# Optimization experiments

Measured on AMD Instinct MI355X. Metric: run time of the kernel, lower is better.

The kernel has to match this reference:

```python
import jax, jax.numpy as jnp
import numpy as np

RCR, RCA = 5.1, 3.5
ETA_R, ZETA, ETA_A = 19.7, 14.1, 12.5
SHF_R = jnp.asarray((0.8 + 0.26875 * np.arange(16)).astype(np.float32))   # 16 radial shifts
SHF_Z = jnp.asarray(((2 * np.arange(8) + 1) * np.pi / 8).astype(np.float32))  # 8 angle shifts
SHF_A = jnp.asarray((0.8 + 0.3375 * np.arange(8)).astype(np.float32))    # 8 angular-radial shifts
NUM_SPECIES = 7
NUM_PAIRS = NUM_SPECIES * (NUM_SPECIES + 1) // 2  # 28 unordered species pairs
N = 2000          # atoms
K = 24            # max neighbors considered for angular terms (Rca=3.5 -> ~18 at this density)
BOX = 27.1        # (N / 0.1 atoms/A^3)^(1/3)

def _triu_index(n):
    ret = np.zeros((n, n), dtype=np.int32)
    iu = np.triu_indices(n)
    ret[iu] = np.arange(iu[0].size)
    ret[iu[1], iu[0]] = ret[iu]
    return ret
TRIU = jnp.asarray(_triu_index(NUM_SPECIES))  # [7,7] -> pair index in 0..27

def _fc(d, rc):
    # cosine cutoff, zero beyond rc
    return jnp.where(d <= rc, 0.5 * jnp.cos(jnp.pi * d / rc) + 0.5, 0.0)

def setup_inputs():
    key = jax.random.key(0)
    k1, k2 = jax.random.split(key)
    species = jax.random.randint(k1, (N,), 0, NUM_SPECIES)
    positions = jax.random.uniform(k2, (N, 3), dtype=jnp.float32) * BOX
    return {"species": species, "positions": positions}

def _aev_mean(species, positions):
    n = positions.shape[0]
    eye = jnp.eye(n, dtype=bool)
    diff = positions[:, None, :] - positions[None, :, :]          # [n,n,3]
    d2 = jnp.sum(diff * diff, -1)
    dist = jnp.sqrt(jnp.where(eye, 1.0, d2))                      # safe sqrt on diagonal
    dist = jnp.where(eye, 2.0 * RCR, dist)                        # exclude self (fc -> 0)

    # ---- radial AEV: 0.25 * exp(-EtaR (d - ShfR)^2) * fc(d, Rcr), scattered by neighbor species
    fc_r = _fc(dist, RCR)
    rad = 0.25 * jnp.exp(-ETA_R * (dist[..., None] - SHF_R) ** 2) * fc_r[..., None]  # [n,n,16]
    oh = jax.nn.one_hot(species, NUM_SPECIES, dtype=positions.dtype)                  # [n,7]
    radial = jnp.einsum('ijr,js->isr', rad, oh)                   # [n,7,16]

    # ---- angular AEV over triplets (j, i, k) with j,k among K nearest neighbors of i
    neg, idx = jax.lax.top_k(-dist, K)                            # idx: [n,K]
    nd = -neg                                                     # neighbor distances [n,K]
    valid = nd <= RCA
    vec = positions[idx] - positions[:, None, :]                  # [n,K,3]
    rj = nd[:, :, None]
    rk = nd[:, None, :]
    cos_ang = 0.95 * jnp.einsum('nad,nbd->nab', vec, vec) / (rj * rk)  # torchani's 0.95 factor
    theta = jnp.arccos(cos_ang)                                   # [n,K,K]
    f1 = ((1.0 + jnp.cos(theta[..., None] - SHF_Z)) / 2.0) ** ZETA               # [n,K,K,8]
    f2 = jnp.exp(-ETA_A * (((rj + rk) / 2.0)[..., None] - SHF_A) ** 2)           # [n,K,K,8]
    fcj = _fc(nd, RCA)
    tri = jnp.triu(jnp.ones((K, K), dtype=bool), 1)               # unordered pairs j<k
    mask = valid[:, :, None] & valid[:, None, :] & tri
    pref = 2.0 * fcj[:, :, None] * fcj[:, None, :] * mask.astype(positions.dtype)
    g = (f1[..., :, None] * f2[..., None, :]).reshape(n, K, K, 64) * pref[..., None]  # [n,K,K,64]
    sp_nb = species[idx]                                          # [n,K]
    pair_idx = TRIU[sp_nb[:, :, None], sp_nb[:, None, :]]         # [n,K,K] in 0..27
    row = jnp.arange(n)[:, None, None]
    angular = jnp.zeros((n, NUM_PAIRS, 64), dtype=positions.dtype).at[row, pair_idx].add(g)

    aev = jnp.concatenate([radial.reshape(n, -1), angular.reshape(n, -1)], axis=-1)  # [n,1904]
    return jnp.mean(aev)

def reference(species, positions):
    return _aev_mean(species, positions)
```

## Files before the change

### kernel.cpp

```cpp
#include <hip/hip_runtime.h>
#include <math.h>

#define NATOMS 2000
#define KNBR   24
#define BLOCK  256
#define NWAVE  4
#define WHCAP  48
#define WACAP  24
#define NFEAT  1904.0f

__device__ __forceinline__ float wave_reduce_add(float v) {
    #pragma unroll
    for (int off = 32; off > 0; off >>= 1) v += __shfl_down(v, off, 64);
    return v;
}

__device__ __forceinline__ int mask_rank_below(unsigned long long m) {
    return (int)__builtin_amdgcn_mbcnt_hi((unsigned)(m >> 32),
                 __builtin_amdgcn_mbcnt_lo((unsigned)m, 0u));
}

__global__ __launch_bounds__(BLOCK) void aev_block_kernel(
        const float* __restrict__ pos, float* __restrict__ partial) {
    constexpr float RCR = 5.1f, RCA = 3.5f;
    constexpr float ETA_R = 19.7f, ZETA = 14.1f, ETA_A = 12.5f;
    constexpr float PI = 3.14159265358979323846f;

    __shared__ float hd2[NWAVE][WHCAP];
    __shared__ int   hj [NWAVE][WHCAP];
    __shared__ float ad [NWAVE][WACAP];
    __shared__ int   aj [NWAVE][WACAP];
    __shared__ int   acnt[NWAVE];
    __shared__ float nbx[KNBR], nby[KNBR], nbz[KNBR], nbd[KNBR], nbfc[KNBR];
    __shared__ float red[NWAVE];

    const int tid  = threadIdx.x;
    const int w    = tid >> 6;
    const int lane = tid & 63;
    const int i    = blockIdx.x;

    const float xi = pos[3 * i + 0], yi = pos[3 * i + 1], zi = pos[3 * i + 2];

    int hbase = 0;
    #pragma unroll 4
    for (int it = 0; it < 8; it++) {
        int j  = w * 64 + it * 256 + lane;
        int jc = j < NATOMS ? j : 0;
        float dx = pos[3 * jc + 0] - xi;
        float dy = pos[3 * jc + 1] - yi;
        float dz = pos[3 * jc + 2] - zi;
        float d2 = dx * dx + dy * dy + dz * dz;
        bool hit = (j < NATOMS) && (j != i) && (d2 <= RCR * RCR);
        unsigned long long m = __ballot(hit);
        if (hit) {
            int idx = hbase + mask_rank_below(m);
            if (idx < WHCAP) { hd2[w][idx] = d2; hj[w][idx] = j; }
        }
        hbase += __popcll(m);
    }

    int hcnt = min(hbase, WHCAP);
    float rsum = 0.0f;
    float d = 0.0f, d2v = 1e9f;
    bool act = lane < hcnt;
    {
        int cl = min(lane, WHCAP - 1);
        if (act) d2v = hd2[w][cl];
        if (act) {
            d = sqrtf(d2v);
            float fc = 0.5f * __cosf(d * (PI / RCR)) + 0.5f;
            float s = 0.0f;
            #pragma unroll
            for (int r = 0; r < 16; r++) {
                float t = d - (0.8f + 0.26875f * (float)r);
                s += __expf(-ETA_R * t * t);
            }
            rsum = 0.25f * fc * s;
        }
        bool ahit = act && (d2v <= RCA * RCA);
        unsigned long long m = __ballot(ahit);
        if (ahit) {
            int idx = mask_rank_below(m);
            if (idx < WACAP) { ad[w][idx] = d; aj[w][idx] = hj[w][min(lane, WHCAP - 1)]; }
        }
        if (lane == 0) acnt[w] = min((int)__popcll(m), WACAP);
    }
    __syncthreads();

    int c0 = acnt[0], c1 = acnt[1], c2 = acnt[2], c3 = acnt[3];
    int cnt = min(c0 + c1 + c2 + c3, 64);
    int M   = min(cnt, KNBR);
    if (tid < cnt) {
        int t = tid, seg = 0;
        if (t >= c0) { t -= c0; seg = 1;
            if (t >= c1) { t -= c1; seg = 2;
                if (t >= c2) { t -= c2; seg = 3; } } }
        float dt = ad[seg][t];
        int   jt = aj[seg][t];
        int rank = 0;
        for (int s = 0; s < NWAVE; s++) {
            int cs = acnt[s];
            for (int u = 0; u < cs; u++) {
                float du = ad[s][u];
                if (du < dt || (du == dt && aj[s][u] < jt)) rank++;
            }
        }
        if (rank < KNBR) {
            nbx[rank]  = pos[3 * jt + 0] - xi;
            nby[rank]  = pos[3 * jt + 1] - yi;
            nbz[rank]  = pos[3 * jt + 2] - zi;
            nbd[rank]  = dt;
            nbfc[rank] = 0.5f * __cosf(dt * (PI / RCA)) + 0.5f;
        }
    }
    __syncthreads();

    const float CZ[4] = { 0.92387953251f, 0.38268343236f, -0.38268343236f, -0.92387953251f };
    const float SZ[4] = { 0.38268343236f, 0.92387953251f,  0.92387953251f,  0.38268343236f };
    float asum = 0.0f;
    int npairs = M * (M - 1) / 2;
    for (int p = tid; p < npairs; p += BLOCK) {
        int a = 0, rem = p;
        while (rem >= M - 1 - a) { rem -= M - 1 - a; a++; }
        int b = a + 1 + rem;

        float ra = nbd[a], rb = nbd[b];
        float dot = nbx[a] * nbx[b] + nby[a] * nby[b] + nbz[a] * nbz[b];
        float ca = 0.95f * dot / (ra * rb);
        float sa = sqrtf(fmaxf(0.0f, 1.0f - ca * ca));

        float f1 = 0.0f;
        #pragma unroll
        for (int z = 0; z < 4; z++) {
            float g = 0.5f * (ca * CZ[z] + sa * SZ[z]);
            f1 += __powf(fmaxf(0.5f + g, 1e-20f), ZETA);
            f1 += __powf(fmaxf(0.5f - g, 1e-20f), ZETA);
        }
        float avg = 0.5f * (ra + rb);
        float f2  = 0.0f;
        #pragma unroll
        for (int s8 = 0; s8 < 8; s8++) {
            float t = avg - (0.8f + 0.3375f * (float)s8);
            f2 += __expf(-ETA_A * t * t);
        }
        asum += 2.0f * nbfc[a] * nbfc[b] * f1 * f2;
    }

    float psum = wave_reduce_add(rsum + asum);
    if (lane == 0) red[w] = psum;
    __syncthreads();
    if (tid == 0) {
        float total = 0.0f;
        #pragma unroll
        for (int q = 0; q < NWAVE; q++) total += red[q];
        partial[i] = total;
    }
}

__global__ __launch_bounds__(BLOCK) void finalize_kernel(
        const float* __restrict__ partial, float* __restrict__ out) {
    __shared__ float red[BLOCK / 64];
    const int tid = threadIdx.x;
    float v = 0.0f;
    for (int c = tid; c < NATOMS; c += BLOCK) v += partial[c];
    v = wave_reduce_add(v);
    if ((tid & 63) == 0) red[tid >> 6] = v;
    __syncthreads();
    if (tid == 0) {
        float total = 0.0f;
        #pragma unroll
        for (int q = 0; q < BLOCK / 64; q++) total += red[q];
        out[0] = total / ((float)NATOMS * NFEAT);
    }
}

extern "C" void kernel_launch(void* const* d_in, const int* in_sizes, int n_in,
                              void* d_out, int out_size, void* d_ws, size_t ws_size,
                              hipStream_t stream) {
    const float* pos = (const float*)d_in[1];
    float* partial = (float*)d_ws;

    aev_block_kernel<<<NATOMS, BLOCK, 0, stream>>>(pos, partial);
    finalize_kernel<<<1, BLOCK, 0, stream>>>(partial, (float*)d_out);
}
```

Baseline: 79.87 us.

## Split neighbor scan into separate wave-parallel kernel with global atomic hit lists

Moves the all-pairs distance scan out of the per-atom block into its own kernel, where eight waves per atom each scan a 256-atom slice and append hits to a global per-atom list through atomics. The AEV kernel then reads the compacted hit list, uses one block-wide list instead of per-wave segments, and ranks angular neighbors over a single array. The intent is to raise parallelism in the scan and simplify the ranking. The cost is an extra memset, an extra launch, and a global round-trip of the hit data. Neighbor order within the hit list now depends on atomic ordering, but ranking breaks ties by index, so the chosen set stays deterministic.

```diff
diff --git a/kernel.cpp b/kernel.cpp
--- a/kernel.cpp
+++ b/kernel.cpp
@@ -4,10 +4,15 @@
 #define NATOMS 2000
 #define KNBR   24
 #define BLOCK  256
-#define NWAVE  4
-#define WHCAP  48
-#define WACAP  24
-#define NFEAT  1904.0f
+#define HCAP   128
+#define ACAP   64
+#define NSUB   8
+#define INV_SCALE (1.0f / (2000.0f * 1904.0f))
+
+__device__ __forceinline__ int mask_rank_below(unsigned long long m) {
+    return (int)__builtin_amdgcn_mbcnt_hi((unsigned)(m >> 32),
+                 __builtin_amdgcn_mbcnt_lo((unsigned)m, 0u));
+}
 
 __device__ __forceinline__ float wave_reduce_add(float v) {
     #pragma unroll
@@ -15,36 +20,21 @@
     return v;
 }
 
-__device__ __forceinline__ int mask_rank_below(unsigned long long m) {
-    return (int)__builtin_amdgcn_mbcnt_hi((unsigned)(m >> 32),
-                 __builtin_amdgcn_mbcnt_lo((unsigned)m, 0u));
-}
-
-__global__ __launch_bounds__(BLOCK) void aev_block_kernel(
-        const float* __restrict__ pos, float* __restrict__ partial) {
-    constexpr float RCR = 5.1f, RCA = 3.5f;
-    constexpr float ETA_R = 19.7f, ZETA = 14.1f, ETA_A = 12.5f;
-    constexpr float PI = 3.14159265358979323846f;
-
-    __shared__ float hd2[NWAVE][WHCAP];
-    __shared__ int   hj [NWAVE][WHCAP];
-    __shared__ float ad [NWAVE][WACAP];
-    __shared__ int   aj [NWAVE][WACAP];
-    __shared__ int   acnt[NWAVE];
-    __shared__ float nbx[KNBR], nby[KNBR], nbz[KNBR], nbd[KNBR], nbfc[KNBR];
-    __shared__ float red[NWAVE];
-
-    const int tid  = threadIdx.x;
-    const int w    = tid >> 6;
-    const int lane = tid & 63;
-    const int i    = blockIdx.x;
+__global__ __launch_bounds__(BLOCK) void scan_kernel(
+        const float* __restrict__ pos, int* __restrict__ cnt,
+        float2* __restrict__ hits) {
+    constexpr float RCR = 5.1f;
+    const int lane = threadIdx.x & 63;
+    int wid = blockIdx.x * (BLOCK / 64) + (threadIdx.x >> 6);
+    wid = __builtin_amdgcn_readfirstlane(wid);
+    const int i   = wid >> 3;
+    const int sub = wid & 7;
 
     const float xi = pos[3 * i + 0], yi = pos[3 * i + 1], zi = pos[3 * i + 2];
 
-    int hbase = 0;
-    #pragma unroll 4
-    for (int it = 0; it < 8; it++) {
-        int j  = w * 64 + it * 256 + lane;
+    #pragma unroll
+    for (int q = 0; q < 4; q++) {
+        int j  = sub * 256 + q * 64 + lane;
         int jc = j < NATOMS ? j : 0;
         float dx = pos[3 * jc + 0] - xi;
         float dy = pos[3 * jc + 1] - yi;
@@ -52,24 +42,51 @@
         float d2 = dx * dx + dy * dy + dz * dz;
         bool hit = (j < NATOMS) && (j != i) && (d2 <= RCR * RCR);
         unsigned long long m = __ballot(hit);
+        int nw = __popcll(m);
+        int base = 0;
+        if (lane == 0 && nw) base = atomicAdd(&cnt[i], nw);
+        base = __shfl(base, 0, 64);
         if (hit) {
-            int idx = hbase + mask_rank_below(m);
-            if (idx < WHCAP) { hd2[w][idx] = d2; hj[w][idx] = j; }
-        }
-        hbase += __popcll(m);
-    }
-
-    int hcnt = min(hbase, WHCAP);
+            int idx = base + mask_rank_below(m);
+            if (idx < HCAP)
+                hits[i * HCAP + idx] = make_float2(sqrtf(d2), __int_as_float(j));
+        }
+    }
+}
+
+__global__ __launch_bounds__(BLOCK) void aev_kernel(
+        const float* __restrict__ pos, const int* __restrict__ cnt,
+        const float2* __restrict__ hits, float* __restrict__ partial) {
+    constexpr float RCR = 5.1f, RCA = 3.5f;
+    constexpr float ETA_R = 19.7f, ZETA = 14.1f, ETA_A = 12.5f;
+    constexpr float PI = 3.14159265358979323846f;
+
+    __shared__ float ad[ACAP];
+    __shared__ int   aj[ACAP];
+    __shared__ int   s_acnt;
+    __shared__ float nbx[KNBR], nby[KNBR], nbz[KNBR], nbd[KNBR], nbfc[KNBR];
+    __shared__ float red[BLOCK / 64];
+
+    const int tid  = threadIdx.x;
+    const int lane = tid & 63;
+    const int i    = blockIdx.x;
+
+    if (tid == 0) s_acnt = 0;
+    __syncthreads();
+
+    const float xi = pos[3 * i + 0], yi = pos[3 * i + 1], zi = pos[3 * i + 2];
+    const int hcnt = min(cnt[i], HCAP);
+
     float rsum = 0.0f;
-    float d = 0.0f, d2v = 1e9f;
-    bool act = lane < hcnt;
     {
-        int cl = min(lane, WHCAP - 1);
-        if (act) d2v = hd2[w][cl];
+        bool act = tid < hcnt;
+        float d = 1.0e9f; int jv = 0;
         if (act) {
-            d = sqrtf(d2v);
+            float2 h = hits[i * HCAP + tid];
+            d  = h.x;
+            jv = __float_as_int(h.y);
             float fc = 0.5f * __cosf(d * (PI / RCR)) + 0.5f;
-            float s = 0.0f;
+            float s  = 0.0f;
             #pragma unroll
             for (int r = 0; r < 16; r++) {
                 float t = d - (0.8f + 0.26875f * (float)r);
@@ -77,33 +94,28 @@
             }
             rsum = 0.25f * fc * s;
         }
-        bool ahit = act && (d2v <= RCA * RCA);
+        bool ahit = act && (d <= RCA);
         unsigned long long m = __ballot(ahit);
+        int nw = __popcll(m);
+        int base = 0;
+        if (lane == 0 && nw) base = atomicAdd(&s_acnt, nw);
+        base = __shfl(base, 0, 64);
         if (ahit) {
-            int idx = mask_rank_below(m);
-            if (idx < WACAP) { ad[w][idx] = d; aj[w][idx] = hj[w][min(lane, WHCAP - 1)]; }
-        }
-        if (lane == 0) acnt[w] = min((int)__popcll(m), WACAP);
-    }
-    __syncthreads();
-
-    int c0 = acnt[0], c1 = acnt[1], c2 = acnt[2], c3 = acnt[3];
-    int cnt = min(c0 + c1 + c2 + c3, 64);
-    int M   = min(cnt, KNBR);
-    if (tid < cnt) {
-        int t = tid, seg = 0;
-        if (t >= c0) { t -= c0; seg = 1;
-            if (t >= c1) { t -= c1; seg = 2;
-                if (t >= c2) { t -= c2; seg = 3; } } }
-        float dt = ad[seg][t];
-        int   jt = aj[seg][t];
+            int idx = base + mask_rank_below(m);
+            if (idx < ACAP) { ad[idx] = d; aj[idx] = jv; }
+        }
+    }
+    __syncthreads();
+
+    int acnt = min(s_acnt, ACAP);
+    int M    = min(acnt, KNBR);
+    if (tid < acnt) {
+        float dt = ad[tid];
+        int   jt = aj[tid];
         int rank = 0;
-        for (int s = 0; s < NWAVE; s++) {
-            int cs = acnt[s];
-            for (int u = 0; u < cs; u++) {
-                float du = ad[s][u];
-                if (du < dt || (du == dt && aj[s][u] < jt)) rank++;
-            }
+        for (int u = 0; u < acnt; u++) {
+            float du = ad[u];
+            if (du < dt || (du == dt && aj[u] < jt)) rank++;
         }
         if (rank < KNBR) {
             nbx[rank]  = pos[3 * jt + 0] - xi;
@@ -147,12 +159,12 @@
     }
 
     float psum = wave_reduce_add(rsum + asum);
-    if (lane == 0) red[w] = psum;
+    if (lane == 0) red[tid >> 6] = psum;
     __syncthreads();
     if (tid == 0) {
         float total = 0.0f;
         #pragma unroll
-        for (int q = 0; q < NWAVE; q++) total += red[q];
+        for (int q = 0; q < BLOCK / 64; q++) total += red[q];
         partial[i] = total;
     }
 }
@@ -170,7 +182,7 @@
         float total = 0.0f;
         #pragma unroll
         for (int q = 0; q < BLOCK / 64; q++) total += red[q];
-        out[0] = total / ((float)NATOMS * NFEAT);
+        out[0] = total * INV_SCALE;
     }
 }
 
@@ -178,8 +190,13 @@
                               void* d_out, int out_size, void* d_ws, size_t ws_size,
                               hipStream_t stream) {
     const float* pos = (const float*)d_in[1];
-    float* partial = (float*)d_ws;
-
-    aev_block_kernel<<<NATOMS, BLOCK, 0, stream>>>(pos, partial);
+
+    int*    cnt     = (int*)d_ws;
+    float2* hits    = (float2*)((char*)d_ws + 8192);
+    float*  partial = (float*)((char*)d_ws + 8192 + (size_t)NATOMS * HCAP * sizeof(float2));
+
+    hipMemsetAsync(cnt, 0, NATOMS * sizeof(int), stream);
+    scan_kernel<<<NATOMS * NSUB / (BLOCK / 64), BLOCK, 0, stream>>>(pos, cnt, hits);
+    aev_kernel<<<NATOMS, BLOCK, 0, stream>>>(pos, cnt, hits, partial);
     finalize_kernel<<<1, BLOCK, 0, stream>>>(partial, (float*)d_out);
 }
```

Result: slower. 96.44 us (+20.8%).

## Process two atoms per block and skip ranking when few angular neighbors

Applied to the files above, without the earlier changes.

Each 512-thread block now handles two atoms, one per 256-thread half. Neighbor displacement vectors are kept in shared memory instead of being re-gathered from global positions. The top-K ranking pass is skipped when the angular candidate count is within K, pair indices are computed in closed form rather than by a loop, and per-wave partials are written directly to remove the block-level reduction. Together these aim to cut global re-reads, serial ranking work and block count, in exchange for higher shared memory use and a larger finalize reduction.

```diff
diff --git a/kernel.cpp b/kernel.cpp
--- a/kernel.cpp
+++ b/kernel.cpp
@@ -3,11 +3,18 @@
 
 #define NATOMS 2000
 #define KNBR   24
-#define BLOCK  256
-#define NWAVE  4
-#define WHCAP  48
-#define WACAP  24
-#define NFEAT  1904.0f
+#define APB    2
+#define BLOCK  512
+#define NBLK   (NATOMS / APB)
+#define RSEG   48
+#define ASEG   24
+#define TMPC   96
+#define INV_SCALE (1.0f / (2000.0f * 1904.0f))
+
+__device__ __forceinline__ int mask_rank_below(unsigned long long m) {
+    return (int)__builtin_amdgcn_mbcnt_hi((unsigned)(m >> 32),
+                 __builtin_amdgcn_mbcnt_lo((unsigned)m, 0u));
+}
 
 __device__ __forceinline__ float wave_reduce_add(float v) {
     #pragma unroll
@@ -15,36 +22,36 @@
     return v;
 }
 
-__device__ __forceinline__ int mask_rank_below(unsigned long long m) {
-    return (int)__builtin_amdgcn_mbcnt_hi((unsigned)(m >> 32),
-                 __builtin_amdgcn_mbcnt_lo((unsigned)m, 0u));
-}
-
-__global__ __launch_bounds__(BLOCK) void aev_block_kernel(
+__global__ __launch_bounds__(BLOCK) void aev_kernel(
         const float* __restrict__ pos, float* __restrict__ partial) {
     constexpr float RCR = 5.1f, RCA = 3.5f;
     constexpr float ETA_R = 19.7f, ZETA = 14.1f, ETA_A = 12.5f;
     constexpr float PI = 3.14159265358979323846f;
 
-    __shared__ float hd2[NWAVE][WHCAP];
-    __shared__ int   hj [NWAVE][WHCAP];
-    __shared__ float ad [NWAVE][WACAP];
-    __shared__ int   aj [NWAVE][WACAP];
-    __shared__ int   acnt[NWAVE];
-    __shared__ float nbx[KNBR], nby[KNBR], nbz[KNBR], nbd[KNBR], nbfc[KNBR];
-    __shared__ float red[NWAVE];
+    __shared__ float rdw[APB][4][RSEG], rxw[APB][4][RSEG],
+                     ryw[APB][4][RSEG], rzw[APB][4][RSEG];
+    __shared__ float qdw[APB][4][ASEG], qxw[APB][4][ASEG],
+                     qyw[APB][4][ASEG], qzw[APB][4][ASEG];
+    __shared__ int   qjw[APB][4][ASEG];
+    __shared__ int   qc[APB][4];
+    __shared__ float td[APB][TMPC], txv[APB][TMPC], tyv[APB][TMPC],
+                     tzv[APB][TMPC], tfc[APB][TMPC];
+    __shared__ int   tj[APB][TMPC];
+    __shared__ float sdv[APB][KNBR], sxv[APB][KNBR], syv[APB][KNBR],
+                     szv[APB][KNBR], sfc[APB][KNBR];
 
     const int tid  = threadIdx.x;
-    const int w    = tid >> 6;
+    const int h    = tid >> 8;
+    const int ht   = tid & 255;
+    const int w    = ht >> 6;
     const int lane = tid & 63;
-    const int i    = blockIdx.x;
+    const int i    = blockIdx.x * APB + h;
 
     const float xi = pos[3 * i + 0], yi = pos[3 * i + 1], zi = pos[3 * i + 2];
 
-    int hbase = 0;
-    #pragma unroll 4
-    for (int it = 0; it < 8; it++) {
-        int j  = w * 64 + it * 256 + lane;
+    int hb = 0;
+    for (int it = 0; it < 8; ++it) {
+        int j  = it * 256 + w * 64 + lane;
         int jc = j < NATOMS ? j : 0;
         float dx = pos[3 * jc + 0] - xi;
         float dy = pos[3 * jc + 1] - yi;
@@ -53,79 +60,102 @@
         bool hit = (j < NATOMS) && (j != i) && (d2 <= RCR * RCR);
         unsigned long long m = __ballot(hit);
         if (hit) {
-            int idx = hbase + mask_rank_below(m);
-            if (idx < WHCAP) { hd2[w][idx] = d2; hj[w][idx] = j; }
-        }
-        hbase += __popcll(m);
-    }
-
-    int hcnt = min(hbase, WHCAP);
+            int idx = hb + mask_rank_below(m);
+            if (idx < RSEG) {
+                rdw[h][w][idx] = sqrtf(d2);
+                rxw[h][w][idx] = dx; ryw[h][w][idx] = dy; rzw[h][w][idx] = dz;
+            }
+        }
+        hb += __popcll(m);
+    }
+    int hc = min(hb, RSEG);
+
     float rsum = 0.0f;
-    float d = 0.0f, d2v = 1e9f;
-    bool act = lane < hcnt;
     {
-        int cl = min(lane, WHCAP - 1);
-        if (act) d2v = hd2[w][cl];
-        if (act) {
-            d = sqrtf(d2v);
-            float fc = 0.5f * __cosf(d * (PI / RCR)) + 0.5f;
-            float s = 0.0f;
-            #pragma unroll
-            for (int r = 0; r < 16; r++) {
-                float t = d - (0.8f + 0.26875f * (float)r);
-                s += __expf(-ETA_R * t * t);
+        bool act = lane < hc;
+        int  cl  = min(lane, RSEG - 1);
+        float d  = act ? rdw[h][w][cl] : 1.0e9f;
+        float fc = 0.5f * __cosf(d * (PI / RCR)) + 0.5f;
+        float s  = 0.0f;
+        #pragma unroll
+        for (int r = 0; r < 16; r++) {
+            float t = d - (0.8f + 0.26875f * (float)r);
+            s += __expf(-ETA_R * t * t);
+        }
+        rsum = act ? 0.25f * fc * s : 0.0f;
+        bool ah = act && (d <= RCA);
+        unsigned long long m = __ballot(ah);
+        if (ah) {
+            int idx = mask_rank_below(m);
+            if (idx < ASEG) {
+                qdw[h][w][idx] = d;
+                qxw[h][w][idx] = rxw[h][w][cl];
+                qyw[h][w][idx] = ryw[h][w][cl];
+                qzw[h][w][idx] = rzw[h][w][cl];
+                qjw[h][w][idx] = 0;
             }
-            rsum = 0.25f * fc * s;
-        }
-        bool ahit = act && (d2v <= RCA * RCA);
-        unsigned long long m = __ballot(ahit);
-        if (ahit) {
-            int idx = mask_rank_below(m);
-            if (idx < WACAP) { ad[w][idx] = d; aj[w][idx] = hj[w][min(lane, WHCAP - 1)]; }
-        }
-        if (lane == 0) acnt[w] = min((int)__popcll(m), WACAP);
-    }
-    __syncthreads();
-
-    int c0 = acnt[0], c1 = acnt[1], c2 = acnt[2], c3 = acnt[3];
-    int cnt = min(c0 + c1 + c2 + c3, 64);
-    int M   = min(cnt, KNBR);
-    if (tid < cnt) {
-        int t = tid, seg = 0;
+        }
+        if (lane == 0) qc[h][w] = min((int)__popcll(m), ASEG);
+    }
+    __syncthreads();
+
+    int c0 = qc[h][0], c1 = qc[h][1], c2 = qc[h][2], c3 = qc[h][3];
+    int cnt = c0 + c1 + c2 + c3;
+    if (ht < cnt) {
+        int t = ht, seg = 0;
         if (t >= c0) { t -= c0; seg = 1;
             if (t >= c1) { t -= c1; seg = 2;
                 if (t >= c2) { t -= c2; seg = 3; } } }
-        float dt = ad[seg][t];
-        int   jt = aj[seg][t];
+        float d = qdw[h][seg][t];
+        td [h][ht] = d;
+        txv[h][ht] = qxw[h][seg][t];
+        tyv[h][ht] = qyw[h][seg][t];
+        tzv[h][ht] = qzw[h][seg][t];
+        tfc[h][ht] = 0.5f * __cosf(d * (PI / RCA)) + 0.5f;
+        tj [h][ht] = ht;
+    }
+    __syncthreads();
+
+    const int M  = min(cnt, KNBR);
+    const bool slow = cnt > KNBR;
+    if (slow && ht < cnt) {
+        float dt = td[h][ht];
+        int   jt = tj[h][ht];
         int rank = 0;
-        for (int s = 0; s < NWAVE; s++) {
-            int cs = acnt[s];
-            for (int u = 0; u < cs; u++) {
-                float du = ad[s][u];
-                if (du < dt || (du == dt && aj[s][u] < jt)) rank++;
-            }
+        for (int u = 0; u < cnt; u++) {
+            float du = td[h][u];
+            if (du < dt || (du == dt && tj[h][u] < jt)) rank++;
         }
         if (rank < KNBR) {
-            nbx[rank]  = pos[3 * jt + 0] - xi;
-            nby[rank]  = pos[3 * jt + 1] - yi;
-            nbz[rank]  = pos[3 * jt + 2] - zi;
-            nbd[rank]  = dt;
-            nbfc[rank] = 0.5f * __cosf(dt * (PI / RCA)) + 0.5f;
-        }
-    }
-    __syncthreads();
+            sdv[h][rank] = dt;
+            sxv[h][rank] = txv[h][ht];
+            syv[h][rank] = tyv[h][ht];
+            szv[h][rank] = tzv[h][ht];
+            sfc[h][rank] = tfc[h][ht];
+        }
+    }
+    __syncthreads();
+
+    const float* Pd = slow ? sdv[h] : td [h];
+    const float* Px = slow ? sxv[h] : txv[h];
+    const float* Py = slow ? syv[h] : tyv[h];
+    const float* Pz = slow ? szv[h] : tzv[h];
+    const float* Pf = slow ? sfc[h] : tfc[h];
 
     const float CZ[4] = { 0.92387953251f, 0.38268343236f, -0.38268343236f, -0.92387953251f };
     const float SZ[4] = { 0.38268343236f, 0.92387953251f,  0.92387953251f,  0.38268343236f };
     float asum = 0.0f;
     int npairs = M * (M - 1) / 2;
-    for (int p = tid; p < npairs; p += BLOCK) {
-        int a = 0, rem = p;
-        while (rem >= M - 1 - a) { rem -= M - 1 - a; a++; }
-        int b = a + 1 + rem;
-
-        float ra = nbd[a], rb = nbd[b];
-        float dot = nbx[a] * nbx[b] + nby[a] * nby[b] + nbz[a] * nbz[b];
+    for (int p = ht; p < npairs; p += 256) {
+        float tm = (float)(2 * M - 1);
+        int a = (int)(0.5f * (tm - sqrtf(fmaxf(0.0f, tm * tm - 8.0f * (float)p))));
+        a = max(0, min(a, M - 2));
+        while (a > 0 && p < (a * (2 * M - 1 - a)) / 2) a--;
+        while (p >= ((a + 1) * (2 * M - 2 - a)) / 2) a++;
+        int b = p - (a * (2 * M - 1 - a)) / 2 + a + 1;
+
+        float ra = Pd[a], rb = Pd[b];
+        float dot = Px[a] * Px[b] + Py[a] * Py[b] + Pz[a] * Pz[b];
         float ca = 0.95f * dot / (ra * rb);
         float sa = sqrtf(fmaxf(0.0f, 1.0f - ca * ca));
 
@@ -143,35 +173,24 @@
             float t = avg - (0.8f + 0.3375f * (float)s8);
             f2 += __expf(-ETA_A * t * t);
         }
-        asum += 2.0f * nbfc[a] * nbfc[b] * f1 * f2;
-    }
-
-    float psum = wave_reduce_add(rsum + asum);
-    if (lane == 0) red[w] = psum;
-    __syncthreads();
-    if (tid == 0) {
-        float total = 0.0f;
-        #pragma unroll
-        for (int q = 0; q < NWAVE; q++) total += red[q];
-        partial[i] = total;
-    }
-}
-
-__global__ __launch_bounds__(BLOCK) void finalize_kernel(
+        asum += 2.0f * Pf[a] * Pf[b] * f1 * f2;
+    }
+
+    float wsum = wave_reduce_add(rsum + asum);
+    if (lane == 0) partial[i * 4 + w] = wsum;
+}
+
+__global__ __launch_bounds__(256) void finalize_kernel(
         const float* __restrict__ partial, float* __restrict__ out) {
-    __shared__ float red[BLOCK / 64];
+    __shared__ float red[4];
     const int tid = threadIdx.x;
     float v = 0.0f;
-    for (int c = tid; c < NATOMS; c += BLOCK) v += partial[c];
+    for (int c = tid; c < NATOMS * 4; c += 256) v += partial[c];
     v = wave_reduce_add(v);
     if ((tid & 63) == 0) red[tid >> 6] = v;
     __syncthreads();
-    if (tid == 0) {
-        float total = 0.0f;
-        #pragma unroll
-        for (int q = 0; q < BLOCK / 64; q++) total += red[q];
-        out[0] = total / ((float)NATOMS * NFEAT);
-    }
+    if (tid == 0)
+        out[0] = (red[0] + red[1] + red[2] + red[3]) * INV_SCALE;
 }
 
 extern "C" void kernel_launch(void* const* d_in, const int* in_sizes, int n_in,
@@ -180,6 +199,6 @@
     const float* pos = (const float*)d_in[1];
     float* partial = (float*)d_ws;
 
-    aev_block_kernel<<<NATOMS, BLOCK, 0, stream>>>(pos, partial);
-    finalize_kernel<<<1, BLOCK, 0, stream>>>(partial, (float*)d_out);
-}
+    aev_kernel<<<NBLK, BLOCK, 0, stream>>>(pos, partial);
+    finalize_kernel<<<1, 256, 0, stream>>>(partial, (float*)d_out);
+}
```

Result: slower. 93.27 us (+16.8%).
